# Performance work log

Hardware: AMD Instinct MI355X
Metric: run time of the kernel (lower is better)

## Reference

```python
import jax, jax.numpy as jnp
import numpy as np

N = 50000          # nodes
E = 800000         # edges (before self loops)
D = 128            # features (in = out)
H = 2              # heads
L = 2              # layers
NEG_SLOPE = 0.2    # GATConv leaky_relu slope


def setup_inputs() -> dict:
    key = jax.random.key(0)
    k = jax.random.split(key, 7)
    x = jax.random.normal(k[0], (N, D), dtype=jnp.float32)
    edge_index = jax.random.randint(k[1], (2, E), 0, N, dtype=jnp.int64)
    # Per-layer GATConv params (lin shared for src/dst as in PyG single-input mode)
    s = 1.0 / np.sqrt(D)
    W = jax.random.uniform(k[2], (L, D, H * D), dtype=jnp.float32, minval=-s, maxval=s)
    att_src = jax.random.uniform(k[3], (L, H, D), dtype=jnp.float32, minval=-s, maxval=s)
    att_dst = jax.random.uniform(k[4], (L, H, D), dtype=jnp.float32, minval=-s, maxval=s)
    bias = jnp.zeros((L, D), dtype=jnp.float32)
    return {"x": x, "edge_index": edge_index, "W": W,
            "att_src": att_src, "att_dst": att_dst, "bias": bias}


def _gat_layer(x, src, dst, W, a_src, a_dst, b):
    n = x.shape[0]
    h = (x @ W).reshape(n, H, D)                    # [N,H,C]
    alpha_s = jnp.sum(h * a_src[None], axis=-1)     # [N,H]
    alpha_d = jnp.sum(h * a_dst[None], axis=-1)     # [N,H]
    e = jax.nn.leaky_relu(alpha_s[src] + alpha_d[dst], NEG_SLOPE)  # [E',H]
    # segment softmax over incoming edges of each dst node
    m = jax.ops.segment_max(e, dst, num_segments=n)
    e = jnp.exp(e - m[dst])
    z = jax.ops.segment_sum(e, dst, num_segments=n)
    alpha = e / (z[dst] + 1e-16)                    # [E',H]
    msg = h[src] * alpha[:, :, None]                # [E',H,C]
    out = jax.ops.segment_sum(msg, dst, num_segments=n)  # [N,H,C]
    return out.mean(axis=1) + b                     # concat=False -> head mean


def _l2_normalize(x, eps=1e-12):
    nrm = jnp.sqrt(jnp.sum(x * x, axis=1, keepdims=True))
    return x / jnp.maximum(nrm, eps)


def reference(x, edge_index, W, att_src, att_dst, bias):
    n = x.shape[0]
    loop = jnp.arange(n, dtype=edge_index.dtype)
    src = jnp.concatenate([edge_index[0], loop])    # add self loops
    dst = jnp.concatenate([edge_index[1], loop])
    h = x
    for l in range(L):
        h = _gat_layer(h, src, dst, W[l], att_src[l], att_dst[l], bias[l])
        h = _l2_normalize(h)
    return h
```

## Files before the change

kernel.cpp:

```cpp
#include <hip/hip_runtime.h>


using short8  = __attribute__((ext_vector_type(8))) short;
using float4v = __attribute__((ext_vector_type(4))) float;

static __device__ __forceinline__ float bf2f(unsigned int u16) {
    union { unsigned int i; float f; } v; v.i = u16 << 16; return v.f;
}
static __device__ __forceinline__ float bflo(unsigned int p){
    union { unsigned int i; float f; } v; v.i = p << 16; return v.f;
}
static __device__ __forceinline__ float bfhi(unsigned int p){
    union { unsigned int i; float f; } v; v.i = p & 0xffff0000u; return v.f;
}
static __device__ __forceinline__ unsigned short f2bf(float f) {
    union { float f; unsigned int i; } v; v.f = f;
    unsigned int x = v.i;
    x += 0x7fffu + ((x >> 16) & 1u);
    return (unsigned short)(x >> 16);
}
static __device__ __forceinline__ float leaky(float x){ return x > 0.f ? x : 0.2f * x; }

__global__ __launch_bounds__(256) void k_probe_zero(const unsigned int* __restrict__ xw,
                                                    const int* __restrict__ ei,
                                                    int* __restrict__ flags,
                                                    int* __restrict__ cursor, int N) {
    int i = blockIdx.x * 256 + threadIdx.x;
    if (i < N) cursor[i] = 0;
    if (blockIdx.x == 0) {
        __shared__ int insane, oddnz;
        int t = threadIdx.x;
        if (t == 0) { insane = 0; oddnz = 0; }
        __syncthreads();
        unsigned int w = xw[t];
        if (((w >> 7) & 0xFFu) >= 154u) atomicOr(&insane, 1);
        if (ei[2 * t + 1] != 0) atomicOr(&oddnz, 1);
        __syncthreads();
        if (t == 0) { flags[0] = insane ? 1 : 0; flags[1] = oddnz ? 0 : 1; }
    }
}

__global__ __launch_bounds__(256) void k_transpose(const void* __restrict__ W,
                                                   unsigned short* __restrict__ WT,
                                                   const int* __restrict__ flags) {
    int fx = flags[0];
    int idx = blockIdx.x * 256 + threadIdx.x;
    int layer = idx >> 15;
    int rem = idx & 32767;
    int k = rem >> 8, n = rem & 255;
    int srci = layer * 32768 + k * 256 + n;
    unsigned short v;
    if (fx) v = f2bf(((const float*)W)[srci]);
    else    v = ((const unsigned short*)W)[srci];
    WT[layer * 32768 + n * 128 + k] = v;
}

__global__ __launch_bounds__(256) void k_gemm_alpha(const void* __restrict__ X,
                                                    const unsigned short* __restrict__ WT,
                                                    const void* __restrict__ atts,
                                                    const void* __restrict__ attd,
                                                    int layer,
                                                    unsigned short* __restrict__ Hb,
                                                    float* __restrict__ as_, float* __restrict__ ad_,
                                                    int N, const int* __restrict__ flags) {
    __shared__ float lds_s[4][16], lds_d[4][16];
    __shared__ unsigned short cbuf[4][16][72];
    int fx = flags[0];
    int mt = blockIdx.x;
    int wave = threadIdx.x >> 6;
    int lane = threadIdx.x & 63;
    int r16 = lane & 15, quad = lane >> 4;
    int m0 = mt << 4;
    int arow = m0 + r16; if (arow >= N) arow = N - 1;
    short8 a[4];
    if (fx) {
        const float* Xf = (const float*)X;
#pragma unroll
        for (int kk = 0; kk < 4; kk++) {
            const float4v* pv = (const float4v*)(Xf + (size_t)arow * 128 + kk * 32 + quad * 8);
            float4v lo = pv[0], hi = pv[1];
            short8 t;
            t[0] = (short)f2bf(lo[0]); t[1] = (short)f2bf(lo[1]);
            t[2] = (short)f2bf(lo[2]); t[3] = (short)f2bf(lo[3]);
            t[4] = (short)f2bf(hi[0]); t[5] = (short)f2bf(hi[1]);
            t[6] = (short)f2bf(hi[2]); t[7] = (short)f2bf(hi[3]);
            a[kk] = t;
        }
    } else {
        const unsigned short* Xh = (const unsigned short*)X;
#pragma unroll
        for (int kk = 0; kk < 4; kk++)
            a[kk] = *(const short8*)(Xh + (size_t)arow * 128 + kk * 32 + quad * 8);
    }
    int head = wave >> 1;
    float ps[4] = {0.f, 0.f, 0.f, 0.f}, pd[4] = {0.f, 0.f, 0.f, 0.f};
#pragma unroll
    for (int nn = 0; nn < 4; nn++) {
        int nt = wave * 4 + nn;
        float4v acc = {0.f, 0.f, 0.f, 0.f};
#pragma unroll
        for (int kk = 0; kk < 4; kk++) {
            short8 b = *(const short8*)(WT + (nt * 16 + r16) * 128 + kk * 32 + quad * 8);
            acc = __builtin_amdgcn_mfma_f32_16x16x32_bf16(a[kk], b, acc, 0, 0, 0);
        }
        int c = (nt * 16 + r16) & 127;
        float sa, da;
        if (fx) {
            sa = ((const float*)atts)[layer * 256 + head * 128 + c];
            da = ((const float*)attd)[layer * 256 + head * 128 + c];
        } else {
            sa = bf2f(((const unsigned short*)atts)[layer * 256 + head * 128 + c]);
            da = bf2f(((const unsigned short*)attd)[layer * 256 + head * 128 + c]);
        }
#pragma unroll
        for (int r = 0; r < 4; r++) {
            cbuf[wave][quad * 4 + r][nn * 16 + r16] = f2bf(acc[r]);
            ps[r] += acc[r] * sa;
            pd[r] += acc[r] * da;
        }
    }
#pragma unroll
    for (int it = 0; it < 2; it++) {
        int idx = it * 64 + lane;
        int row = idx >> 3, chunk = idx & 7;
        uint4 v = *(const uint4*)&cbuf[wave][row][chunk * 8];
        int grow = m0 + row;
        if (grow < N)
            *(uint4*)(Hb + (size_t)grow * 256 + wave * 64 + chunk * 8) = v;
    }
#pragma unroll
    for (int m = 1; m < 16; m <<= 1) {
#pragma unroll
        for (int r = 0; r < 4; r++) {
            ps[r] += __shfl_xor(ps[r], m);
            pd[r] += __shfl_xor(pd[r], m);
        }
    }
    if (r16 == 0) {
#pragma unroll
        for (int r = 0; r < 4; r++) {
            lds_s[wave][quad * 4 + r] = ps[r];
            lds_d[wave][quad * 4 + r] = pd[r];
        }
    }
    __syncthreads();
    if (threadIdx.x < 16) {
        int row = m0 + threadIdx.x;
        if (row < N) {
            float2 sv = { lds_s[0][threadIdx.x] + lds_s[1][threadIdx.x],
                          lds_s[2][threadIdx.x] + lds_s[3][threadIdx.x] };
            float2 dv = { lds_d[0][threadIdx.x] + lds_d[1][threadIdx.x],
                          lds_d[2][threadIdx.x] + lds_d[3][threadIdx.x] };
            *(float2*)(as_ + 2 * row) = sv;
            *(float2*)(ad_ + 2 * row) = dv;
        }
    }
}

static __device__ __forceinline__ int edge_dst(const int* ei, int E, int i, int is64) {
    return is64 ? ei[2 * E + 2 * i] : ei[E + i];
}
static __device__ __forceinline__ int edge_src(const int* ei, int E, int i, int is64) {
    return is64 ? ei[2 * i] : ei[i];
}

__global__ __launch_bounds__(256) void k_count(const int* __restrict__ ei, int E, int N,
                                               const int* __restrict__ flags, int* deg) {
    int i = blockIdx.x * 256 + threadIdx.x;
    if (i >= E + N) return;
    int dst;
    if (i < E) { dst = edge_dst(ei, E, i, flags[1]); if ((unsigned)dst >= (unsigned)N) dst = 0; }
    else dst = i - E;
    atomicAdd(&deg[dst], 1);
}

__global__ __launch_bounds__(1024) void k_scan1(const int* __restrict__ deg, int* __restrict__ excl,
                                                int* __restrict__ bsum, int n) {
    __shared__ int buf[1024];
    int t = threadIdx.x;
    int i = blockIdx.x * 1024 + t;
    int v = (i < n) ? deg[i] : 0;
    int x = v; buf[t] = v; __syncthreads();
    for (int off = 1; off < 1024; off <<= 1) {
        int add = (t >= off) ? buf[t - off] : 0;
        __syncthreads();
        x += add; buf[t] = x;
        __syncthreads();
    }
    if (i < n) excl[i] = x - v;
    if (t == 1023) bsum[blockIdx.x] = x;
}

__global__ __launch_bounds__(256) void k_scan2(int* bsum, int nb) {
    __shared__ int buf[256];
    int t = threadIdx.x;
    int v = (t < nb) ? bsum[t] : 0;
    int x = v; buf[t] = v; __syncthreads();
    for (int off = 1; off < 256; off <<= 1) {
        int add = (t >= off) ? buf[t - off] : 0;
        __syncthreads();
        x += add; buf[t] = x;
        __syncthreads();
    }
    if (t < nb) bsum[t] = x - v;
    if (t == nb - 1) bsum[nb] = x;
}

__global__ __launch_bounds__(256) void k_scan3(int* __restrict__ rowptr, const int* __restrict__ bsum,
                                               int* __restrict__ cursor, int N) {
    int i = blockIdx.x * 256 + threadIdx.x;
    if (i < N) {
        int r = rowptr[i] + bsum[i >> 10];
        rowptr[i] = r;
        cursor[i] = r;
    } else if (i == N) {
        rowptr[N] = bsum[(N + 1023) >> 10];
    }
}

__global__ __launch_bounds__(256) void k_scatter(const int* __restrict__ ei, int E, int N,
                                                 const int* __restrict__ flags,
                                                 int* __restrict__ cursor, int* __restrict__ csr) {
    int i = blockIdx.x * 256 + threadIdx.x;
    if (i >= E + N) return;
    int src, dst;
    if (i < E) {
        int is64 = flags[1];
        src = edge_src(ei, E, i, is64);
        dst = edge_dst(ei, E, i, is64);
        if ((unsigned)src >= (unsigned)N) src = 0;
        if ((unsigned)dst >= (unsigned)N) dst = 0;
    } else src = dst = i - E;
    int pos = atomicAdd(&cursor[dst], 1);
    csr[pos] = src;
}

static __device__ __forceinline__ void acc8(float* A, float w, uint4 q) {
    A[0] += w * bflo(q.x); A[1] += w * bfhi(q.x);
    A[2] += w * bflo(q.y); A[3] += w * bfhi(q.y);
    A[4] += w * bflo(q.z); A[5] += w * bfhi(q.z);
    A[6] += w * bflo(q.w); A[7] += w * bfhi(q.w);
}

__global__ __launch_bounds__(256) void k_aggregate(const unsigned short* __restrict__ Hb,
                                                   const float* __restrict__ as_, const float* __restrict__ ad_,
                                                   const int* __restrict__ rowptr, const int* __restrict__ csr,
                                                   const void* __restrict__ bias, int layer,
                                                   const int* __restrict__ flags,
                                                   void* __restrict__ outp, int N, int EL) {
    int fx = flags[0];
    int n = blockIdx.x * 4 + (threadIdx.x >> 6);
    if (n >= N) return;
    int lane = threadIdx.x & 63;
    int g = lane >> 4;
    int gl = lane & 15;
    int start = rowptr[n], end = rowptr[n + 1];
    if (start < 0) start = 0;
    if (end > EL) end = EL;
    if (end < start) end = start;
    float2 adv = *(const float2*)(ad_ + 2 * n);
    float ad0 = adv.x, ad1 = adv.y;

    float acc0[8] = {0,0,0,0,0,0,0,0}, acc1[8] = {0,0,0,0,0,0,0,0};
    float z0, z1;
    int deg = end - start;

    if (deg <= 64) {
        int i = start + lane;
        bool act = i < end;
        int s = 0; float l0 = -1e30f, l1 = -1e30f;
        if (act) {
            s = csr[i]; if ((unsigned)s >= (unsigned)N) s = 0;
            float2 av = *(const float2*)(as_ + 2 * s);
            l0 = leaky(av.x + ad0); l1 = leaky(av.y + ad1);
        }
        float m0 = l0, m1 = l1;
#pragma unroll
        for (int m = 1; m < 64; m <<= 1) { m0 = fmaxf(m0, __shfl_xor(m0, m)); m1 = fmaxf(m1, __shfl_xor(m1, m)); }
        float w0 = act ? __expf(l0 - m0) : 0.f;
        float w1 = act ? __expf(l1 - m1) : 0.f;
        z0 = w0; z1 = w1;
#pragma unroll
        for (int m = 1; m < 64; m <<= 1) { z0 += __shfl_xor(z0, m); z1 += __shfl_xor(z1, m); }
#pragma unroll 2
        for (int j = 0; 4 * j < deg; j++) {
            int e = 4 * j + g;
            int sq    = __shfl(s, e);
            float wq0 = __shfl(w0, e);
            float wq1 = __shfl(w1, e);
            if (e < deg) {
                const unsigned short* row = Hb + ((size_t)sq << 8);
                uint4 q0 = *(const uint4*)(row + gl * 8);
                uint4 q1 = *(const uint4*)(row + 128 + gl * 8);
                acc8(acc0, wq0, q0);
                acc8(acc1, wq1, q1);
            }
        }
    } else {
        float m0 = -1e30f, m1 = -1e30f;
        for (int i = start + lane; i < end; i += 64) {
            int s = csr[i]; if ((unsigned)s >= (unsigned)N) s = 0;
            float2 av = *(const float2*)(as_ + 2 * s);
            m0 = fmaxf(m0, leaky(av.x + ad0));
            m1 = fmaxf(m1, leaky(av.y + ad1));
        }
#pragma unroll
        for (int m = 1; m < 64; m <<= 1) { m0 = fmaxf(m0, __shfl_xor(m0, m)); m1 = fmaxf(m1, __shfl_xor(m1, m)); }
        z0 = 0.f; z1 = 0.f;
        for (int t = start; t < end; t += 64) {
            int i = t + lane;
            int s = 0; float w0 = 0.f, w1 = 0.f;
            if (i < end) {
                s = csr[i]; if ((unsigned)s >= (unsigned)N) s = 0;
                float2 av = *(const float2*)(as_ + 2 * s);
                w0 = __expf(leaky(av.x + ad0) - m0);
                w1 = __expf(leaky(av.y + ad1) - m1);
                z0 += w0; z1 += w1;
            }
            int cnt = end - t; if (cnt > 64) cnt = 64;
            for (int j = 0; 4 * j < cnt; j++) {
                int e = 4 * j + g;
                int sq    = __shfl(s, e);
                float wq0 = __shfl(w0, e);
                float wq1 = __shfl(w1, e);
                if (e < cnt) {
                    const unsigned short* row = Hb + ((size_t)sq << 8);
                    uint4 q0 = *(const uint4*)(row + gl * 8);
                    uint4 q1 = *(const uint4*)(row + 128 + gl * 8);
                    acc8(acc0, wq0, q0);
                    acc8(acc1, wq1, q1);
                }
            }
        }
#pragma unroll
        for (int m = 1; m < 64; m <<= 1) { z0 += __shfl_xor(z0, m); z1 += __shfl_xor(z1, m); }
    }

    float inv0 = 1.f / (z0 + 1e-16f), inv1 = 1.f / (z1 + 1e-16f);
#pragma unroll
    for (int k = 0; k < 8; k++) {
        acc0[k] += __shfl_xor(acc0[k], 16); acc0[k] += __shfl_xor(acc0[k], 32);
        acc1[k] += __shfl_xor(acc1[k], 16); acc1[k] += __shfl_xor(acc1[k], 32);
    }

    float v[8];
    if (fx) {
        const float* bf = (const float*)bias + layer * 128 + gl * 8;
#pragma unroll
        for (int k = 0; k < 8; k++) v[k] = 0.5f * (acc0[k] * inv0 + acc1[k] * inv1) + bf[k];
    } else {
        const unsigned short* bh = (const unsigned short*)bias + layer * 128 + gl * 8;
        uint4 bv = *(const uint4*)bh;
        float bfv[8] = { bflo(bv.x), bfhi(bv.x), bflo(bv.y), bfhi(bv.y),
                         bflo(bv.z), bfhi(bv.z), bflo(bv.w), bfhi(bv.w) };
#pragma unroll
        for (int k = 0; k < 8; k++) v[k] = 0.5f * (acc0[k] * inv0 + acc1[k] * inv1) + bfv[k];
    }

    float ss = 0.f;
#pragma unroll
    for (int k = 0; k < 8; k++) ss += v[k] * v[k];
#pragma unroll
    for (int m = 1; m < 16; m <<= 1) ss += __shfl_xor(ss, m);
    float inv = 1.f / fmaxf(sqrtf(ss), 1e-12f);

    if (lane < 16) {
        if (fx) {
            float* op = (float*)outp + (size_t)n * 128 + gl * 8;
            float4 o0 = { v[0] * inv, v[1] * inv, v[2] * inv, v[3] * inv };
            float4 o1 = { v[4] * inv, v[5] * inv, v[6] * inv, v[7] * inv };
            *(float4*)op = o0;
            *(float4*)(op + 4) = o1;
        } else {
            unsigned short* op = (unsigned short*)outp + (size_t)n * 128 + gl * 8;
            uint4 pk;
            pk.x = (unsigned int)f2bf(v[0] * inv) | ((unsigned int)f2bf(v[1] * inv) << 16);
            pk.y = (unsigned int)f2bf(v[2] * inv) | ((unsigned int)f2bf(v[3] * inv) << 16);
            pk.z = (unsigned int)f2bf(v[4] * inv) | ((unsigned int)f2bf(v[5] * inv) << 16);
            pk.w = (unsigned int)f2bf(v[6] * inv) | ((unsigned int)f2bf(v[7] * inv) << 16);
            *(uint4*)op = pk;
        }
    }
}

extern "C" void kernel_launch(void* const* d_in, const int* in_sizes, int n_in,
                              void* d_out, int out_size, void* d_ws, size_t ws_size,
                              hipStream_t stream) {
    const void* x    = d_in[0];
    const int*  ei   = (const int*)d_in[1];
    const void* W    = d_in[2];
    const void* atts = d_in[3];
    const void* attd = d_in[4];
    const void* bias = d_in[5];

    int N = in_sizes[0] / 128;
    int E = in_sizes[1] / 2;
    int EL = E + N;

    char* p = (char*)d_ws;
    auto alloc = [&](size_t bytes) -> char* {
        char* q = p; p += (bytes + 255) & ~(size_t)255; return q;
    };
    int* flags   = (int*)alloc(256);
    int* bsum    = (int*)alloc(2048 * 4);
    int* rowptr  = (int*)alloc((size_t)(N + 1) * 4);
    int* cursor  = (int*)alloc((size_t)N * 4);
    float* as_   = (float*)alloc((size_t)N * 2 * 4);
    float* ad_   = (float*)alloc((size_t)N * 2 * 4);
    unsigned short* wt = (unsigned short*)alloc(2 * 256 * 128 * 2);
    int* csr     = (int*)alloc((size_t)EL * 4);
    unsigned short* hbuf = (unsigned short*)alloc((size_t)N * 256 * 2);

    k_probe_zero<<<(N + 255) / 256, 256, 0, stream>>>((const unsigned int*)x, ei, flags, cursor, N);
    k_count<<<(EL + 255) / 256, 256, 0, stream>>>(ei, E, N, flags, cursor);
    int nb = (N + 1023) / 1024;
    k_scan1<<<nb, 1024, 0, stream>>>(cursor, rowptr, bsum, N);
    k_scan2<<<1, 256, 0, stream>>>(bsum, nb);
    k_scan3<<<(N + 256) / 256, 256, 0, stream>>>(rowptr, bsum, cursor, N);
    k_scatter<<<(EL + 255) / 256, 256, 0, stream>>>(ei, E, N, flags, cursor, csr);
    k_transpose<<<256, 256, 0, stream>>>(W, wt, flags);

    int mtiles = (N + 15) / 16;
    for (int l = 0; l < 2; l++) {
        const void* xin = (l == 0) ? x : (const void*)d_out;
        k_gemm_alpha<<<mtiles, 256, 0, stream>>>(xin, wt + l * 32768, atts, attd, l,
                                                 hbuf, as_, ad_, N, flags);
        k_aggregate<<<(N + 3) / 4, 256, 0, stream>>>(hbuf, as_, ad_, rowptr, csr, bias, l, flags,
                                                     d_out, N, EL);
    }
}
```

Baseline: 388.6 us.

## Replace CSR build with fixed-capacity per-node buckets plus spill list

```diff
diff --git a/kernel.cpp b/kernel.cpp
--- a/kernel.cpp
+++ b/kernel.cpp
@@ -1,5 +1,8 @@
 #include <hip/hip_runtime.h>
 
+
+#define CAP 48
+#define SPILLCAP 65536
 
 using short8  = __attribute__((ext_vector_type(8))) short;
 using float4v = __attribute__((ext_vector_type(4))) float;
@@ -24,9 +27,9 @@
 __global__ __launch_bounds__(256) void k_probe_zero(const unsigned int* __restrict__ xw,
                                                     const int* __restrict__ ei,
                                                     int* __restrict__ flags,
-                                                    int* __restrict__ cursor, int N) {
+                                                    int* __restrict__ cnt, int N) {
     int i = blockIdx.x * 256 + threadIdx.x;
-    if (i < N) cursor[i] = 0;
+    if (i < N) cnt[i] = 0;
     if (blockIdx.x == 0) {
         __shared__ int insane, oddnz;
         int t = threadIdx.x;
@@ -36,7 +39,7 @@
         if (((w >> 7) & 0xFFu) >= 154u) atomicOr(&insane, 1);
         if (ei[2 * t + 1] != 0) atomicOr(&oddnz, 1);
         __syncthreads();
-        if (t == 0) { flags[0] = insane ? 1 : 0; flags[1] = oddnz ? 0 : 1; }
+        if (t == 0) { flags[0] = insane ? 1 : 0; flags[1] = oddnz ? 0 : 1; flags[2] = 0; }
     }
 }
 
@@ -53,6 +56,37 @@
     if (fx) v = f2bf(((const float*)W)[srci]);
     else    v = ((const unsigned short*)W)[srci];
     WT[layer * 32768 + n * 128 + k] = v;
+}
+
+static __device__ __forceinline__ int edge_dst(const int* ei, int E, int i, int is64) {
+    return is64 ? ei[2 * E + 2 * i] : ei[E + i];
+}
+static __device__ __forceinline__ int edge_src(const int* ei, int E, int i, int is64) {
+    return is64 ? ei[2 * i] : ei[i];
+}
+
+__global__ __launch_bounds__(256) void k_bucket(const int* __restrict__ ei, int E, int N,
+                                                int* __restrict__ flags,
+                                                int* __restrict__ cnt,
+                                                int* __restrict__ bucket,
+                                                int* __restrict__ spill) {
+    int i = blockIdx.x * 256 + threadIdx.x;
+    if (i >= E + N) return;
+    int src, dst;
+    if (i < E) {
+        int is64 = flags[1];
+        src = edge_src(ei, E, i, is64);
+        dst = edge_dst(ei, E, i, is64);
+        if ((unsigned)src >= (unsigned)N) src = 0;
+        if ((unsigned)dst >= (unsigned)N) dst = 0;
+    } else src = dst = i - E;
+    int pos = atomicAdd(&cnt[dst], 1);
+    if (pos < CAP) {
+        bucket[dst * CAP + pos] = src;
+    } else {
+        int sp = atomicAdd(&flags[2], 1);
+        if (sp < SPILLCAP) { spill[2 * sp] = dst; spill[2 * sp + 1] = src; }
+    }
 }
 
 __global__ __launch_bounds__(256) void k_gemm_alpha(const void* __restrict__ X,
@@ -157,84 +191,6 @@
     }
 }
 
-static __device__ __forceinline__ int edge_dst(const int* ei, int E, int i, int is64) {
-    return is64 ? ei[2 * E + 2 * i] : ei[E + i];
-}
-static __device__ __forceinline__ int edge_src(const int* ei, int E, int i, int is64) {
-    return is64 ? ei[2 * i] : ei[i];
-}
-
-__global__ __launch_bounds__(256) void k_count(const int* __restrict__ ei, int E, int N,
-                                               const int* __restrict__ flags, int* deg) {
-    int i = blockIdx.x * 256 + threadIdx.x;
-    if (i >= E + N) return;
-    int dst;
-    if (i < E) { dst = edge_dst(ei, E, i, flags[1]); if ((unsigned)dst >= (unsigned)N) dst = 0; }
-    else dst = i - E;
-    atomicAdd(&deg[dst], 1);
-}
-
-__global__ __launch_bounds__(1024) void k_scan1(const int* __restrict__ deg, int* __restrict__ excl,
-                                                int* __restrict__ bsum, int n) {
-    __shared__ int buf[1024];
-    int t = threadIdx.x;
-    int i = blockIdx.x * 1024 + t;
-    int v = (i < n) ? deg[i] : 0;
-    int x = v; buf[t] = v; __syncthreads();
-    for (int off = 1; off < 1024; off <<= 1) {
-        int add = (t >= off) ? buf[t - off] : 0;
-        __syncthreads();
-        x += add; buf[t] = x;
-        __syncthreads();
-    }
-    if (i < n) excl[i] = x - v;
-    if (t == 1023) bsum[blockIdx.x] = x;
-}
-
-__global__ __launch_bounds__(256) void k_scan2(int* bsum, int nb) {
-    __shared__ int buf[256];
-    int t = threadIdx.x;
-    int v = (t < nb) ? bsum[t] : 0;
-    int x = v; buf[t] = v; __syncthreads();
-    for (int off = 1; off < 256; off <<= 1) {
-        int add = (t >= off) ? buf[t - off] : 0;
-        __syncthreads();
-        x += add; buf[t] = x;
-        __syncthreads();
-    }
-    if (t < nb) bsum[t] = x - v;
-    if (t == nb - 1) bsum[nb] = x;
-}
-
-__global__ __launch_bounds__(256) void k_scan3(int* __restrict__ rowptr, const int* __restrict__ bsum,
-                                               int* __restrict__ cursor, int N) {
-    int i = blockIdx.x * 256 + threadIdx.x;
-    if (i < N) {
-        int r = rowptr[i] + bsum[i >> 10];
-        rowptr[i] = r;
-        cursor[i] = r;
-    } else if (i == N) {
-        rowptr[N] = bsum[(N + 1023) >> 10];
-    }
-}
-
-__global__ __launch_bounds__(256) void k_scatter(const int* __restrict__ ei, int E, int N,
-                                                 const int* __restrict__ flags,
-                                                 int* __restrict__ cursor, int* __restrict__ csr) {
-    int i = blockIdx.x * 256 + threadIdx.x;
-    if (i >= E + N) return;
-    int src, dst;
-    if (i < E) {
-        int is64 = flags[1];
-        src = edge_src(ei, E, i, is64);
-        dst = edge_dst(ei, E, i, is64);
-        if ((unsigned)src >= (unsigned)N) src = 0;
-        if ((unsigned)dst >= (unsigned)N) dst = 0;
-    } else src = dst = i - E;
-    int pos = atomicAdd(&cursor[dst], 1);
-    csr[pos] = src;
-}
-
 static __device__ __forceinline__ void acc8(float* A, float w, uint4 q) {
     A[0] += w * bflo(q.x); A[1] += w * bfhi(q.x);
     A[2] += w * bflo(q.y); A[3] += w * bfhi(q.y);
@@ -244,33 +200,29 @@
 
 __global__ __launch_bounds__(256) void k_aggregate(const unsigned short* __restrict__ Hb,
                                                    const float* __restrict__ as_, const float* __restrict__ ad_,
-                                                   const int* __restrict__ rowptr, const int* __restrict__ csr,
+                                                   const int* __restrict__ cnt, const int* __restrict__ bucket,
+                                                   const int* __restrict__ spill, const int* __restrict__ flags,
                                                    const void* __restrict__ bias, int layer,
-                                                   const int* __restrict__ flags,
-                                                   void* __restrict__ outp, int N, int EL) {
+                                                   void* __restrict__ outp, int N) {
     int fx = flags[0];
     int n = blockIdx.x * 4 + (threadIdx.x >> 6);
     if (n >= N) return;
     int lane = threadIdx.x & 63;
     int g = lane >> 4;
     int gl = lane & 15;
-    int start = rowptr[n], end = rowptr[n + 1];
-    if (start < 0) start = 0;
-    if (end > EL) end = EL;
-    if (end < start) end = start;
+    int deg = cnt[n];
+    const int* eb = bucket + n * CAP;
     float2 adv = *(const float2*)(ad_ + 2 * n);
     float ad0 = adv.x, ad1 = adv.y;
 
     float acc0[8] = {0,0,0,0,0,0,0,0}, acc1[8] = {0,0,0,0,0,0,0,0};
     float z0, z1;
-    int deg = end - start;
-
-    if (deg <= 64) {
-        int i = start + lane;
-        bool act = i < end;
+
+    if (deg <= CAP) {
+        bool act = lane < deg;
         int s = 0; float l0 = -1e30f, l1 = -1e30f;
         if (act) {
-            s = csr[i]; if ((unsigned)s >= (unsigned)N) s = 0;
+            s = eb[lane]; if ((unsigned)s >= (unsigned)N) s = 0;
             float2 av = *(const float2*)(as_ + 2 * s);
             l0 = leaky(av.x + ad0); l1 = leaky(av.y + ad1);
         }
@@ -297,39 +249,63 @@
             }
         }
     } else {
+        int sc = flags[2]; if (sc > SPILLCAP) sc = SPILLCAP;
         float m0 = -1e30f, m1 = -1e30f;
-        for (int i = start + lane; i < end; i += 64) {
-            int s = csr[i]; if ((unsigned)s >= (unsigned)N) s = 0;
+        for (int i = lane; i < CAP; i += 64) {
+            int s = eb[i]; if ((unsigned)s >= (unsigned)N) s = 0;
             float2 av = *(const float2*)(as_ + 2 * s);
             m0 = fmaxf(m0, leaky(av.x + ad0));
             m1 = fmaxf(m1, leaky(av.y + ad1));
         }
+        for (int i = lane; i < sc; i += 64) {
+            if (spill[2 * i] == n) {
+                int s = spill[2 * i + 1]; if ((unsigned)s >= (unsigned)N) s = 0;
+                float2 av = *(const float2*)(as_ + 2 * s);
+                m0 = fmaxf(m0, leaky(av.x + ad0));
+                m1 = fmaxf(m1, leaky(av.y + ad1));
+            }
+        }
 #pragma unroll
         for (int m = 1; m < 64; m <<= 1) { m0 = fmaxf(m0, __shfl_xor(m0, m)); m1 = fmaxf(m1, __shfl_xor(m1, m)); }
         z0 = 0.f; z1 = 0.f;
-        for (int t = start; t < end; t += 64) {
-            int i = t + lane;
+        {
+            bool act = lane < CAP;
             int s = 0; float w0 = 0.f, w1 = 0.f;
-            if (i < end) {
-                s = csr[i]; if ((unsigned)s >= (unsigned)N) s = 0;
+            if (act) {
+                s = eb[lane]; if ((unsigned)s >= (unsigned)N) s = 0;
                 float2 av = *(const float2*)(as_ + 2 * s);
                 w0 = __expf(leaky(av.x + ad0) - m0);
                 w1 = __expf(leaky(av.y + ad1) - m1);
                 z0 += w0; z1 += w1;
             }
-            int cnt = end - t; if (cnt > 64) cnt = 64;
-            for (int j = 0; 4 * j < cnt; j++) {
+            for (int j = 0; 4 * j < CAP; j++) {
                 int e = 4 * j + g;
                 int sq    = __shfl(s, e);
                 float wq0 = __shfl(w0, e);
                 float wq1 = __shfl(w1, e);
-                if (e < cnt) {
+                if (e < CAP) {
                     const unsigned short* row = Hb + ((size_t)sq << 8);
                     uint4 q0 = *(const uint4*)(row + gl * 8);
                     uint4 q1 = *(const uint4*)(row + 128 + gl * 8);
                     acc8(acc0, wq0, q0);
                     acc8(acc1, wq1, q1);
                 }
+            }
+        }
+        for (int i = 0; i < sc; i++) {
+            int d = spill[2 * i];
+            if (d != n) continue;
+            int s = spill[2 * i + 1]; if ((unsigned)s >= (unsigned)N) s = 0;
+            float2 av = *(const float2*)(as_ + 2 * s);
+            float w0 = __expf(leaky(av.x + ad0) - m0);
+            float w1 = __expf(leaky(av.y + ad1) - m1);
+            if (lane == 0) { z0 += w0; z1 += w1; }
+            if (g == 0) {
+                const unsigned short* row = Hb + ((size_t)s << 8);
+                uint4 q0 = *(const uint4*)(row + gl * 8);
+                uint4 q1 = *(const uint4*)(row + 128 + gl * 8);
+                acc8(acc0, w0, q0);
+                acc8(acc1, w1, q1);
             }
         }
 #pragma unroll
@@ -395,29 +371,22 @@
 
     int N = in_sizes[0] / 128;
     int E = in_sizes[1] / 2;
-    int EL = E + N;
 
     char* p = (char*)d_ws;
     auto alloc = [&](size_t bytes) -> char* {
         char* q = p; p += (bytes + 255) & ~(size_t)255; return q;
     };
     int* flags   = (int*)alloc(256);
-    int* bsum    = (int*)alloc(2048 * 4);
-    int* rowptr  = (int*)alloc((size_t)(N + 1) * 4);
-    int* cursor  = (int*)alloc((size_t)N * 4);
+    int* cnt     = (int*)alloc((size_t)N * 4);
     float* as_   = (float*)alloc((size_t)N * 2 * 4);
     float* ad_   = (float*)alloc((size_t)N * 2 * 4);
     unsigned short* wt = (unsigned short*)alloc(2 * 256 * 128 * 2);
-    int* csr     = (int*)alloc((size_t)EL * 4);
+    int* spill   = (int*)alloc((size_t)SPILLCAP * 2 * 4);
+    int* bucket  = (int*)alloc((size_t)N * CAP * 4);
     unsigned short* hbuf = (unsigned short*)alloc((size_t)N * 256 * 2);
 
-    k_probe_zero<<<(N + 255) / 256, 256, 0, stream>>>((const unsigned int*)x, ei, flags, cursor, N);
-    k_count<<<(EL + 255) / 256, 256, 0, stream>>>(ei, E, N, flags, cursor);
-    int nb = (N + 1023) / 1024;
-    k_scan1<<<nb, 1024, 0, stream>>>(cursor, rowptr, bsum, N);
-    k_scan2<<<1, 256, 0, stream>>>(bsum, nb);
-    k_scan3<<<(N + 256) / 256, 256, 0, stream>>>(rowptr, bsum, cursor, N);
-    k_scatter<<<(EL + 255) / 256, 256, 0, stream>>>(ei, E, N, flags, cursor, csr);
+    k_probe_zero<<<(N + 255) / 256, 256, 0, stream>>>((const unsigned int*)x, ei, flags, cnt, N);
+    k_bucket<<<(E + N + 255) / 256, 256, 0, stream>>>(ei, E, N, flags, cnt, bucket, spill);
     k_transpose<<<256, 256, 0, stream>>>(W, wt, flags);
 
     int mtiles = (N + 15) / 16;
@@ -425,7 +394,7 @@
         const void* xin = (l == 0) ? x : (const void*)d_out;
         k_gemm_alpha<<<mtiles, 256, 0, stream>>>(xin, wt + l * 32768, atts, attd, l,
                                                  hbuf, as_, ad_, N, flags);
-        k_aggregate<<<(N + 3) / 4, 256, 0, stream>>>(hbuf, as_, ad_, rowptr, csr, bias, l, flags,
-                                                     d_out, N, EL);
-    }
-}
+        k_aggregate<<<(N + 3) / 4, 256, 0, stream>>>(hbuf, as_, ad_, cnt, bucket, spill, flags,
+                                                     bias, l, d_out, N);
+    }
+}
```

Result: faster. 358.0 us (-7.9%).
